# Kernel optimization log

Measured on AMD Instinct MI355X. Metric: run time of the kernel, lower is better.

Reference implementation:

```python
import jax, jax.numpy as jnp
import numpy as np

N = 50000      # nodes
E = 800000     # edges (before self-loops)
IN = 256       # input_dim
H = 8          # heads (hard-coded in module)
C = 32         # hidden_dim per head
OUT = 64       # output_dim
NEG_SLOPE = 0.2  # PyG GATConv default leaky_relu slope


def setup_inputs() -> dict:
    key = jax.random.key(0)
    ks = jax.random.split(key, 8)
    x = jax.random.normal(ks[0], (N, IN), dtype=jnp.float32)
    edge_index = jax.random.randint(ks[1], (2, E), 0, N, dtype=jnp.int64)
    # GATConv params (concat=True -> out width H*C)
    W_gat = jax.random.normal(ks[2], (IN, H * C), dtype=jnp.float32) * (1.0 / np.sqrt(IN))
    att_src = jax.random.normal(ks[3], (1, H, C), dtype=jnp.float32) * (1.0 / np.sqrt(C))
    att_dst = jax.random.normal(ks[4], (1, H, C), dtype=jnp.float32) * (1.0 / np.sqrt(C))
    bias_gat = jnp.zeros((H * C,), dtype=jnp.float32)
    # final Linear
    W_lin = jax.random.normal(ks[5], (H * C, OUT), dtype=jnp.float32) * (1.0 / np.sqrt(H * C))
    b_lin = jnp.zeros((OUT,), dtype=jnp.float32)
    return {"x": x, "edge_index": edge_index, "W_gat": W_gat, "att_src": att_src,
            "att_dst": att_dst, "bias_gat": bias_gat, "W_lin": W_lin, "b_lin": b_lin}


def reference(x, edge_index, W_gat, att_src, att_dst, bias_gat, W_lin, b_lin):
    # add self-loops (PyG GATConv default add_self_loops=True)
    ar = jnp.arange(N, dtype=edge_index.dtype)
    ei = jnp.concatenate([edge_index, jnp.stack([ar, ar])], axis=1)  # [2, E+N]
    src, dst = ei[0], ei[1]

    h = (x @ W_gat).reshape(N, H, C)                # [N,H,C]
    a_src = jnp.sum(h * att_src, axis=-1)           # [N,H]
    a_dst = jnp.sum(h * att_dst, axis=-1)           # [N,H]

    e = a_src[src] + a_dst[dst]                     # [E+N,H] per-edge logits
    e = jnp.where(e > 0, e, NEG_SLOPE * e)          # leaky_relu

    # segment softmax over incoming edges of each dst node
    m = jax.ops.segment_max(e, dst, num_segments=N)           # [N,H]
    ex = jnp.exp(e - m[dst])                                   # [E+N,H]
    denom = jax.ops.segment_sum(ex, dst, num_segments=N)       # [N,H]
    alpha = ex / (denom[dst] + 1e-16)                           # [E+N,H]

    msg = h[src] * alpha[:, :, None]                            # [E+N,H,C]
    out = jax.ops.segment_sum(msg, dst, num_segments=N)        # [N,H,C]
    out = out.reshape(N, H * C) + bias_gat                      # concat heads + bias

    out = jax.nn.relu(out)
    return out @ W_lin + b_lin                                  # [N,OUT]
```

## Files before the change

### kernel.cpp

```cpp
#include <hip/hip_runtime.h>
#include <hip/hip_bf16.h>

typedef __attribute__((ext_vector_type(8))) short short8v;
typedef __attribute__((ext_vector_type(4))) float floatx4;

__device__ __forceinline__ unsigned short f2bf(float f) {
    unsigned b = __float_as_uint(f);
    b = (b + 0x7fffu + ((b >> 16) & 1u)) >> 16;
    return (unsigned short)b;
}
__device__ __forceinline__ float b2f(unsigned short u) {
    return __uint_as_float((unsigned)u << 16);
}

__global__ void k_prep(const float* __restrict__ s0, unsigned short* __restrict__ d0, int n0,
                       const float* __restrict__ s1, unsigned short* __restrict__ d1, int n1,
                       const float* __restrict__ s2, unsigned short* __restrict__ d2, int n2,
                       const int* __restrict__ ei, int* __restrict__ cnt, int E, int EE) {
    int nconv = n0 + n1 + n2;
    int total = nconv + EE;
    int i = blockIdx.x * blockDim.x + threadIdx.x;
    int stride = gridDim.x * blockDim.x;
    for (; i < total; i += stride) {
        if (i < nconv) {
            const float* s; unsigned short* d; int j;
            if (i < n0) { s = s0; d = d0; j = i; }
            else if (i < n0 + n1) { s = s1; d = d1; j = i - n0; }
            else { s = s2; d = d2; j = i - n0 - n1; }
            float4 v = reinterpret_cast<const float4*>(s)[j];
            ushort4 o;
            o.x = f2bf(v.x); o.y = f2bf(v.y); o.z = f2bf(v.z); o.w = f2bf(v.w);
            reinterpret_cast<ushort4*>(d)[j] = o;
        } else {
            int e = i - nconv;
            int dst = (e < E) ? ei[E + e] : e - E;
            atomicAdd(&cnt[dst], 1);
        }
    }
}

__launch_bounds__(256)
__global__ void k_gemm1(const unsigned short* __restrict__ A,
                        const unsigned short* __restrict__ B,
                        const float* __restrict__ att_src, const float* __restrict__ att_dst,
                        unsigned short* __restrict__ hb,
                        float* __restrict__ a_src, float* __restrict__ a_dst, int M) {
    __shared__ unsigned short BsT[64 * 264];
    const int tid = threadIdx.x;
    const int nt = blockIdx.y;
    const int tM = blockIdx.x * 64;

    for (int it = 0; it < 8; ++it) {
        int f8 = it * 256 + tid;
        int k = f8 >> 3;
        int c0 = (f8 & 7) * 8;
        short8v v = *reinterpret_cast<const short8v*>(B + (size_t)k * 256 + nt * 64 + c0);
#pragma unroll
        for (int j = 0; j < 8; ++j)
            BsT[(c0 + j) * 264 + k] = (unsigned short)v[j];
    }
    __syncthreads();

    const int w  = tid >> 6;
    const int l  = tid & 63;
    const int lg = l >> 4;
    const int lr = l & 15;

    floatx4 acc[4] = {};
    int rowA = tM + w * 16 + lr;
    if (rowA > M - 1) rowA = M - 1;
    const unsigned short* Arow = A + (size_t)rowA * 256 + lg * 8;

#pragma unroll
    for (int kt = 0; kt < 8; ++kt) {
        short8v av = *reinterpret_cast<const short8v*>(Arow + kt * 32);
#pragma unroll
        for (int n = 0; n < 4; ++n) {
            short8v bv = *reinterpret_cast<const short8v*>(&BsT[(n * 16 + lr) * 264 + kt * 32 + lg * 8]);
            acc[n] = __builtin_amdgcn_mfma_f32_16x16x32_bf16(av, bv, acc[n], 0, 0, 0);
        }
    }

    float ps[2][4] = {}, pd[2][4] = {};
#pragma unroll
    for (int n = 0; n < 4; ++n) {
        int hd2 = n >> 1;
        float asv = att_src[(nt * 2 + hd2) * 32 + (n & 1) * 16 + lr];
        float adv = att_dst[(nt * 2 + hd2) * 32 + (n & 1) * 16 + lr];
        int col = nt * 64 + n * 16 + lr;
#pragma unroll
        for (int r = 0; r < 4; ++r) {
            int row = tM + w * 16 + lg * 4 + r;
            float v = acc[n][r];
            if (row < M) hb[(size_t)row * 256 + col] = f2bf(v);
            ps[hd2][r] += v * asv;
            pd[hd2][r] += v * adv;
        }
    }
#pragma unroll
    for (int off = 1; off < 16; off <<= 1) {
#pragma unroll
        for (int hd2 = 0; hd2 < 2; ++hd2)
#pragma unroll
            for (int r = 0; r < 4; ++r) {
                ps[hd2][r] += __shfl_xor(ps[hd2][r], off, 64);
                pd[hd2][r] += __shfl_xor(pd[hd2][r], off, 64);
            }
    }
    if (lr == 0) {
#pragma unroll
        for (int hd2 = 0; hd2 < 2; ++hd2)
#pragma unroll
            for (int r = 0; r < 4; ++r) {
                int row = tM + w * 16 + lg * 4 + r;
                if (row < M) {
                    a_src[(size_t)row * 8 + nt * 2 + hd2] = ps[hd2][r];
                    a_dst[(size_t)row * 8 + nt * 2 + hd2] = pd[hd2][r];
                }
            }
    }
}

__launch_bounds__(256)
__global__ void k_gemm(const unsigned short* __restrict__ A,
                       const unsigned short* __restrict__ B,
                       float* __restrict__ C,
                       const float* __restrict__ bias,
                       int M, int NC) {
    __shared__ unsigned short BsT[64 * 264];
    const int tid = threadIdx.x;
    const int ntile = blockIdx.y;
    const int tM = blockIdx.x * 64;

    for (int it = 0; it < 8; ++it) {
        int f8 = it * 256 + tid;
        int k = f8 >> 3;
        int c0 = (f8 & 7) * 8;
        short8v v = *reinterpret_cast<const short8v*>(B + (size_t)k * NC + ntile * 64 + c0);
#pragma unroll
        for (int j = 0; j < 8; ++j)
            BsT[(c0 + j) * 264 + k] = (unsigned short)v[j];
    }
    __syncthreads();

    const int w  = tid >> 6;
    const int l  = tid & 63;
    const int lg = l >> 4;
    const int lr = l & 15;

    floatx4 acc[4] = {};
    int rowA = tM + w * 16 + lr;
    if (rowA > M - 1) rowA = M - 1;
    const unsigned short* Arow = A + (size_t)rowA * 256 + lg * 8;

#pragma unroll
    for (int kt = 0; kt < 8; ++kt) {
        short8v av = *reinterpret_cast<const short8v*>(Arow + kt * 32);
#pragma unroll
        for (int n = 0; n < 4; ++n) {
            short8v bv = *reinterpret_cast<const short8v*>(&BsT[(n * 16 + lr) * 264 + kt * 32 + lg * 8]);
            acc[n] = __builtin_amdgcn_mfma_f32_16x16x32_bf16(av, bv, acc[n], 0, 0, 0);
        }
    }
#pragma unroll
    for (int n = 0; n < 4; ++n) {
        int col = ntile * 64 + n * 16 + lr;
        float badd = bias ? bias[col] : 0.0f;
#pragma unroll
        for (int r = 0; r < 4; ++r) {
            int row = tM + w * 16 + lg * 4 + r;
            if (row < M) C[(size_t)row * NC + col] = acc[n][r] + badd;
        }
    }
}

#define SCAN_NB 256
__launch_bounds__(256)
__global__ void k_scan_a(const int* __restrict__ cnt, int* __restrict__ bsum, int N) {
    __shared__ int sh[256];
    int b = blockIdx.x, t = threadIdx.x;
    int chunk = (N + SCAN_NB - 1) / SCAN_NB;
    int idx = b * chunk + t;
    sh[t] = (t < chunk && idx < N) ? cnt[idx] : 0;
    __syncthreads();
    for (int off = 128; off > 0; off >>= 1) {
        if (t < off) sh[t] += sh[t + off];
        __syncthreads();
    }
    if (t == 0) bsum[b] = sh[0];
}
__launch_bounds__(256)
__global__ void k_scan_bc(const int* __restrict__ cnt, const int* __restrict__ bsum,
                          int* __restrict__ row_start, int* __restrict__ cursor, int N) {
    __shared__ int shb[256];
    __shared__ int sh[256];
    int b = blockIdx.x, t = threadIdx.x;
    shb[t] = bsum[t];
    __syncthreads();
    for (int off = 1; off < 256; off <<= 1) {
        int v = (t >= off) ? shb[t - off] : 0;
        __syncthreads();
        shb[t] += v;
        __syncthreads();
    }
    int boff = (b == 0) ? 0 : shb[b - 1];

    int chunk = (N + SCAN_NB - 1) / SCAN_NB;
    int idx = b * chunk + t;
    int v = (t < chunk && idx < N) ? cnt[idx] : 0;
    sh[t] = v;
    __syncthreads();
    for (int off = 1; off < 256; off <<= 1) {
        int u = (t >= off) ? sh[t - off] : 0;
        __syncthreads();
        sh[t] += u;
        __syncthreads();
    }
    if (t < chunk && idx < N) {
        int ex = boff + sh[t] - v;
        row_start[idx] = ex;
        cursor[idx] = ex;
    }
}

__global__ void k_scatter(const int* __restrict__ ei, int* __restrict__ cursor,
                          int* __restrict__ sorted_src, int E, int EE) {
    int e = blockIdx.x * blockDim.x + threadIdx.x;
    if (e >= EE) return;
    int src, dst;
    if (e < E) { src = ei[e]; dst = ei[E + e]; } else { src = dst = e - E; }
    int pos = atomicAdd(&cursor[dst], 1);
    sorted_src[pos] = src;
}

__launch_bounds__(256)
__global__ void k_agg(const int* __restrict__ row_start, const int* __restrict__ row_end,
                      const int* __restrict__ sorted_src,
                      const float* __restrict__ a_src, const float* __restrict__ a_dst,
                      const unsigned short* __restrict__ hb,
                      const float* __restrict__ bias_gat,
                      unsigned short* __restrict__ gb, int N) {
    int n = blockIdx.x * 4 + (threadIdx.x >> 6);
    if (n >= N) return;
    int lane = threadIdx.x & 63;
    int hd = lane >> 3;
    int start = row_start[n], end = row_end[n];
    float ad = a_dst[(size_t)n * 8 + hd];
    float ax = 0.f, ay = 0.f, az = 0.f, aw = 0.f, den = 0.f;
    float bx = 0.f, by = 0.f, bz = 0.f, bw = 0.f, den2 = 0.f;
    for (int j0 = start; j0 < end; j0 += 64) {
        int idx = j0 + lane;
        int sv = (idx < end) ? sorted_src[idx] : 0;
        int cnt = end - j0; if (cnt > 64) cnt = 64;
        int jj = 0;
        for (; jj + 3 < cnt; jj += 4) {
            int s0 = __shfl(sv, jj);
            int s1 = __shfl(sv, jj + 1);
            int s2 = __shfl(sv, jj + 2);
            int s3 = __shfl(sv, jj + 3);
            float v0 = a_src[(size_t)s0 * 8 + hd] + ad;
            float v1 = a_src[(size_t)s1 * 8 + hd] + ad;
            float v2 = a_src[(size_t)s2 * 8 + hd] + ad;
            float v3 = a_src[(size_t)s3 * 8 + hd] + ad;
            ushort4 h0 = *reinterpret_cast<const ushort4*>(hb + (size_t)s0 * 256 + lane * 4);
            ushort4 h1 = *reinterpret_cast<const ushort4*>(hb + (size_t)s1 * 256 + lane * 4);
            ushort4 h2 = *reinterpret_cast<const ushort4*>(hb + (size_t)s2 * 256 + lane * 4);
            ushort4 h3 = *reinterpret_cast<const ushort4*>(hb + (size_t)s3 * 256 + lane * 4);
            v0 = v0 > 0.f ? v0 : 0.2f * v0;
            v1 = v1 > 0.f ? v1 : 0.2f * v1;
            v2 = v2 > 0.f ? v2 : 0.2f * v2;
            v3 = v3 > 0.f ? v3 : 0.2f * v3;
            float e0 = __expf(v0), e1 = __expf(v1), e2 = __expf(v2), e3 = __expf(v3);
            den  += e0 + e2; den2 += e1 + e3;
            ax += e0 * b2f(h0.x); ay += e0 * b2f(h0.y);
            az += e0 * b2f(h0.z); aw += e0 * b2f(h0.w);
            bx += e1 * b2f(h1.x); by += e1 * b2f(h1.y);
            bz += e1 * b2f(h1.z); bw += e1 * b2f(h1.w);
            ax += e2 * b2f(h2.x); ay += e2 * b2f(h2.y);
            az += e2 * b2f(h2.z); aw += e2 * b2f(h2.w);
            bx += e3 * b2f(h3.x); by += e3 * b2f(h3.y);
            bz += e3 * b2f(h3.z); bw += e3 * b2f(h3.w);
        }
        for (; jj < cnt; ++jj) {
            int s0 = __shfl(sv, jj);
            float v0 = a_src[(size_t)s0 * 8 + hd] + ad;
            v0 = v0 > 0.f ? v0 : 0.2f * v0;
            float e0 = __expf(v0);
            ushort4 h0 = *reinterpret_cast<const ushort4*>(hb + (size_t)s0 * 256 + lane * 4);
            den += e0;
            ax += e0 * b2f(h0.x); ay += e0 * b2f(h0.y);
            az += e0 * b2f(h0.z); aw += e0 * b2f(h0.w);
        }
    }
    float inv = 1.0f / (den + den2 + 1e-16f);
    float4 b4 = *reinterpret_cast<const float4*>(bias_gat + lane * 4);
    ushort4 o;
    o.x = f2bf(fmaxf((ax + bx) * inv + b4.x, 0.f));
    o.y = f2bf(fmaxf((ay + by) * inv + b4.y, 0.f));
    o.z = f2bf(fmaxf((az + bz) * inv + b4.z, 0.f));
    o.w = f2bf(fmaxf((aw + bw) * inv + b4.w, 0.f));
    reinterpret_cast<ushort4*>(gb)[(size_t)n * 64 + lane] = o;
}

extern "C" void kernel_launch(void* const* d_in, const int* in_sizes, int n_in,
                              void* d_out, int out_size, void* d_ws, size_t ws_size,
                              hipStream_t stream) {
    const float* x        = (const float*)d_in[0];
    const int*   ei       = (const int*)d_in[1];
    const float* W_gat    = (const float*)d_in[2];
    const float* att_src  = (const float*)d_in[3];
    const float* att_dst  = (const float*)d_in[4];
    const float* bias_gat = (const float*)d_in[5];
    const float* W_lin    = (const float*)d_in[6];
    const float* b_lin    = (const float*)d_in[7];
    float* out = (float*)d_out;

    const int N  = in_sizes[0] / 256;
    const int E  = in_sizes[1] / 2;
    const int EE = E + N;

    char* ws = (char*)d_ws;
    size_t off = 0;
    auto alloc = [&](size_t bytes) -> void* {
        void* p = ws + off;
        off = (off + bytes + 255) & ~(size_t)255;
        return p;
    };
    unsigned short* hb       = (unsigned short*)alloc((size_t)N * 256 * 2);
    float*          a_srcv   = (float*)alloc((size_t)N * 8 * 4);
    float*          a_dstv   = (float*)alloc((size_t)N * 8 * 4);
    int*            cnt      = (int*)alloc((size_t)N * 4);
    int*            rowst    = (int*)alloc((size_t)N * 4);
    int*            cursor   = (int*)alloc((size_t)N * 4);
    int*            bsum     = (int*)alloc(SCAN_NB * 4);
    int*            ssrc     = (int*)alloc((size_t)EE * 4);
    unsigned short* xb       = (unsigned short*)alloc((size_t)N * 256 * 2);
    unsigned short* wb       = (unsigned short*)alloc(256 * 256 * 2);
    unsigned short* wlb      = (unsigned short*)alloc(256 * 64 * 2);

    hipMemsetAsync(cnt, 0, (size_t)N * 4, stream);

    k_prep<<<2048, 256, 0, stream>>>(x, xb, N * 256 / 4,
                                     W_gat, wb, 256 * 256 / 4,
                                     W_lin, wlb, 256 * 64 / 4,
                                     ei, cnt, E, EE);

    k_scan_a<<<SCAN_NB, 256, 0, stream>>>(cnt, bsum, N);
    k_scan_bc<<<SCAN_NB, 256, 0, stream>>>(cnt, bsum, rowst, cursor, N);
    k_scatter<<<(EE + 255) / 256, 256, 0, stream>>>(ei, cursor, ssrc, E, EE);

    dim3 g1((N + 63) / 64, 4);
    k_gemm1<<<g1, 256, 0, stream>>>(xb, wb, att_src, att_dst, hb, a_srcv, a_dstv, N);

    k_agg<<<(N + 3) / 4, 256, 0, stream>>>(rowst, cursor, ssrc, a_srcv, a_dstv, hb,
                                           bias_gat, xb, N);

    dim3 g2((N + 63) / 64, 1);
    k_gemm<<<g2, 256, 0, stream>>>(xb, wlb, out, b_lin, N, 64);
}
```

Measured before the change: 236.0 us.

## Fuse edge scatter into GEMM1 launch and XOR-swizzle LDS B tile

Merges the edge scatter kernel and the first GEMM into one launch, with extra trailing blocks doing the CSR scatter while the GEMM blocks run. This removes a launch and lets the latency-bound atomic scatter overlap with the MFMA work. It also applies an XOR swizzle to the transposed B tile in shared memory in both GEMMs to reduce LDS bank conflicts. The combined kernel still reserves the large shared-memory tile for the scatter blocks, which may limit how many of them run at once.

After: 220.4 us. 1.07x faster.

```diff
diff --git a/kernel.cpp b/kernel.cpp
--- a/kernel.cpp
+++ b/kernel.cpp
@@ -12,6 +12,8 @@
 __device__ __forceinline__ float b2f(unsigned short u) {
     return __uint_as_float((unsigned)u << 16);
 }
+
+#define BIDX(col, k) ((col) * 264 + ((k) ^ ((((col) >> 3) & 7) << 3)))
 
 __global__ void k_prep(const float* __restrict__ s0, unsigned short* __restrict__ d0, int n0,
                        const float* __restrict__ s1, unsigned short* __restrict__ d1, int n1,
@@ -40,15 +42,28 @@
 }
 
 __launch_bounds__(256)
-__global__ void k_gemm1(const unsigned short* __restrict__ A,
-                        const unsigned short* __restrict__ B,
-                        const float* __restrict__ att_src, const float* __restrict__ att_dst,
-                        unsigned short* __restrict__ hb,
-                        float* __restrict__ a_src, float* __restrict__ a_dst, int M) {
+__global__ void k_gs(const unsigned short* __restrict__ A,
+                     const unsigned short* __restrict__ B,
+                     const float* __restrict__ att_src, const float* __restrict__ att_dst,
+                     unsigned short* __restrict__ hb,
+                     float* __restrict__ a_src, float* __restrict__ a_dst,
+                     int M, int RB, int GB1,
+                     const int* __restrict__ ei, int* __restrict__ cursor,
+                     int* __restrict__ sorted_src, int E, int EE) {
     __shared__ unsigned short BsT[64 * 264];
+    const int b = blockIdx.x;
+    if (b >= GB1) {
+        int e = (b - GB1) * 256 + threadIdx.x;
+        if (e >= EE) return;
+        int src, dst;
+        if (e < E) { src = ei[e]; dst = ei[E + e]; } else { src = dst = e - E; }
+        int pos = atomicAdd(&cursor[dst], 1);
+        sorted_src[pos] = src;
+        return;
+    }
     const int tid = threadIdx.x;
-    const int nt = blockIdx.y;
-    const int tM = blockIdx.x * 64;
+    const int nt = b / RB;
+    const int tM = (b - nt * RB) * 64;
 
     for (int it = 0; it < 8; ++it) {
         int f8 = it * 256 + tid;
@@ -57,7 +72,7 @@
         short8v v = *reinterpret_cast<const short8v*>(B + (size_t)k * 256 + nt * 64 + c0);
 #pragma unroll
         for (int j = 0; j < 8; ++j)
-            BsT[(c0 + j) * 264 + k] = (unsigned short)v[j];
+            BsT[BIDX(c0 + j, k)] = (unsigned short)v[j];
     }
     __syncthreads();
 
@@ -76,7 +91,7 @@
         short8v av = *reinterpret_cast<const short8v*>(Arow + kt * 32);
 #pragma unroll
         for (int n = 0; n < 4; ++n) {
-            short8v bv = *reinterpret_cast<const short8v*>(&BsT[(n * 16 + lr) * 264 + kt * 32 + lg * 8]);
+            short8v bv = *reinterpret_cast<const short8v*>(&BsT[BIDX(n * 16 + lr, kt * 32 + lg * 8)]);
             acc[n] = __builtin_amdgcn_mfma_f32_16x16x32_bf16(av, bv, acc[n], 0, 0, 0);
         }
     }
@@ -139,7 +154,7 @@
         short8v v = *reinterpret_cast<const short8v*>(B + (size_t)k * NC + ntile * 64 + c0);
 #pragma unroll
         for (int j = 0; j < 8; ++j)
-            BsT[(c0 + j) * 264 + k] = (unsigned short)v[j];
+            BsT[BIDX(c0 + j, k)] = (unsigned short)v[j];
     }
     __syncthreads();
 
@@ -158,7 +173,7 @@
         short8v av = *reinterpret_cast<const short8v*>(Arow + kt * 32);
 #pragma unroll
         for (int n = 0; n < 4; ++n) {
-            short8v bv = *reinterpret_cast<const short8v*>(&BsT[(n * 16 + lr) * 264 + kt * 32 + lg * 8]);
+            short8v bv = *reinterpret_cast<const short8v*>(&BsT[BIDX(n * 16 + lr, kt * 32 + lg * 8)]);
             acc[n] = __builtin_amdgcn_mfma_f32_16x16x32_bf16(av, bv, acc[n], 0, 0, 0);
         }
     }
@@ -221,16 +236,6 @@
         row_start[idx] = ex;
         cursor[idx] = ex;
     }
-}
-
-__global__ void k_scatter(const int* __restrict__ ei, int* __restrict__ cursor,
-                          int* __restrict__ sorted_src, int E, int EE) {
-    int e = blockIdx.x * blockDim.x + threadIdx.x;
-    if (e >= EE) return;
-    int src, dst;
-    if (e < E) { src = ei[e]; dst = ei[E + e]; } else { src = dst = e - E; }
-    int pos = atomicAdd(&cursor[dst], 1);
-    sorted_src[pos] = src;
 }
 
 __launch_bounds__(256)
@@ -347,10 +352,12 @@
 
     k_scan_a<<<SCAN_NB, 256, 0, stream>>>(cnt, bsum, N);
     k_scan_bc<<<SCAN_NB, 256, 0, stream>>>(cnt, bsum, rowst, cursor, N);
-    k_scatter<<<(EE + 255) / 256, 256, 0, stream>>>(ei, cursor, ssrc, E, EE);
-
-    dim3 g1((N + 63) / 64, 4);
-    k_gemm1<<<g1, 256, 0, stream>>>(xb, wb, att_src, att_dst, hb, a_srcv, a_dstv, N);
+
+    const int RB  = (N + 63) / 64;
+    const int GB1 = RB * 4;
+    const int SB  = (EE + 255) / 256;
+    k_gs<<<GB1 + SB, 256, 0, stream>>>(xb, wb, att_src, att_dst, hb, a_srcv, a_dstv,
+                                       N, RB, GB1, ei, cursor, ssrc, E, EE);
 
     k_agg<<<(N + 3) / 4, 256, 0, stream>>>(rowst, cursor, ssrc, a_srcv, a_dstv, hb,
                                            bias_gat, xb, N);
```
